# Optimization experiments

Measured on AMD Instinct MI355X. Metric: run time of the kernel, lower is better.

## Reference

```python
import jax, jax.numpy as jnp
import numpy as np

T, B, HIMG = 16, 1024, 32
VALUE_DIM, KEY_DIM, HIDDEN, OUT_DIM = 64, 64, 512, 4


def _conv(x, w):
    # torch Conv2d(kernel=4, stride=2, padding=0)
    return jax.lax.conv_general_dilated(
        x, w, (2, 2), 'VALID', dimension_numbers=('NCHW', 'OIHW', 'NCHW'))


def setup_inputs() -> dict:
    key = jax.random.key(0)
    ks = jax.random.split(key, 24)

    def w(k, shape, s=0.05):
        return jax.random.normal(k, shape, jnp.float32) * s

    return {
        'images': jax.random.normal(ks[0], (T, B, 3, HIMG, HIMG), jnp.float32),
        # encoder
        'W1': w(ks[1], (32, 3, 4, 4)), 'b1': w(ks[2], (32,)),
        'W2': w(ks[3], (64, 32, 4, 4)), 'b2': w(ks[4], (64,)),
        'W3': w(ks[5], (64, 64, 4, 4)), 'b3': w(ks[6], (64,)),
        'We': w(ks[7], (VALUE_DIM, 4 * 64)), 'be': w(ks[8], (VALUE_DIM,)),
        # LSTMCell(key_dim+1 -> hidden), torch layout (4H, in) / (4H, H)
        'Wih': w(ks[9], (4 * HIDDEN, KEY_DIM + 1)),
        'Whh': w(ks[10], (4 * HIDDEN, HIDDEN)),
        'bih': w(ks[11], (4 * HIDDEN,)), 'bhh': w(ks[12], (4 * HIDDEN,)),
        # heads
        'Wg': w(ks[13], (1, HIDDEN)), 'bg': w(ks[14], (1,)),
        'Wk': w(ks[15], (KEY_DIM, HIDDEN)), 'bk': w(ks[16], (KEY_DIM,)),
        'Wo': w(ks[17], (OUT_DIM, HIDDEN)), 'bo': w(ks[18], (OUT_DIM,)),
        'Wc': w(ks[19], (1, 1)), 'bc': w(ks[20], (1,)),
    }


def _forward(images, W1, b1, W2, b2, W3, b3, We, be,
             Wih, Whh, bih, bhh, Wg, bg, Wk, bk, Wo, bo, Wc, bc):
    t, b = images.shape[0], images.shape[1]

    # Encoder over all frames at once (vectorized over T*B).
    # FAITHFULNESS NOTE: in the source module, the retrieved key `kr` is computed
    # but never assigned back to `kx` (kx stays k0 = zeros after step 0), so the
    # encoder output z / memory banks Mk, Mv / gate / key / confidence heads never
    # influence the returned output. We compute z here to mirror the source; it is
    # dead w.r.t. the output (XLA will DCE it under jit), exactly matching torch.
    x = images.reshape((t * b,) + images.shape[2:])
    h = jax.nn.relu(_conv(x, W1) + b1[None, :, None, None])
    h = jax.nn.relu(_conv(h, W2) + b2[None, :, None, None])
    h = jax.nn.relu(_conv(h, W3) + b3[None, :, None, None])
    z = h.reshape(t * b, -1) @ We.T + be  # (t*b, value_dim) -- dead path
    del z

    hidden = Whh.shape[1]
    kx = jnp.zeros((b, Wih.shape[1]), images.dtype)  # k0; constant every step (source bug)
    const_gates = kx @ Wih.T + bih + bhh             # (b, 4*hidden), hoisted out of the loop

    def step(carry, _):
        hx, cx = carry
        gates = const_gates + hx @ Whh.T
        i, f, g, o = jnp.split(gates, 4, axis=-1)  # torch LSTMCell gate order i,f,g,o
        cx = jax.nn.sigmoid(f) * cx + jax.nn.sigmoid(i) * jnp.tanh(g)
        hx = jax.nn.sigmoid(o) * jnp.tanh(cx)
        return (hx, cx), hx

    init = (jnp.zeros((b, hidden), images.dtype),
            jnp.zeros((b, hidden), images.dtype))
    _, hs = jax.lax.scan(step, init, None, length=t)  # (t, b, hidden)
    return hs @ Wo.T + bo  # (t, b, output_dim) == torch.stack(out)


def reference(images, W1, b1, W2, b2, W3, b3, We, be,
              Wih, Whh, bih, bhh, Wg, bg, Wk, bk, Wo, bo, Wc, bc):
    return _forward(images, W1, b1, W2, b2, W3, b3, We, be,
                    Wih, Whh, bih, bhh, Wg, bg, Wk, bk, Wo, bo, Wc, bc)
```

## Files before the change

kernel.cpp:

```cpp
#include <hip/hip_runtime.h>


#define NTHR   512
#define HID    512
#define TSTEPS 16
#define KPB    16
#define OUTB   16
#define NWORK  32
#define SW     516

typedef unsigned long long ull;

#define LOG2E  1.44269504f

__device__ __forceinline__ float fexp2(float x) { return __builtin_amdgcn_exp2f(x); }
__device__ __forceinline__ float frcp(float x)  { return __builtin_amdgcn_rcpf(x); }
__device__ __forceinline__ float sigm(float x)  { return frcp(1.0f + fexp2(-LOG2E * x)); }
__device__ __forceinline__ float tanh_f(float x) {
  const float e = fexp2(2.0f * LOG2E * x);
  return 1.0f - 2.0f * frcp(e + 1.0f);
}

__device__ __forceinline__ ull probe_l2(const ull* p) {
  ull v;
  asm volatile("global_load_dwordx2 %0, %1, off sc0\n\ts_waitcnt vmcnt(0)"
               : "=v"(v) : "v"(p) : "memory");
  return v;
}

__device__ __forceinline__ float poll_h(const ull* sL2, const ull* sLLC,
                                        int idx, unsigned tag, bool fast) {
  ull v;
  if (fast) {
    for (;;) {
      v = probe_l2(sL2 + idx);
      if ((unsigned)(v >> 32) == tag) break;
      v = __hip_atomic_load(sLLC + idx, __ATOMIC_RELAXED,
                            __HIP_MEMORY_SCOPE_AGENT);
      if ((unsigned)(v >> 32) == tag) break;
    }
  } else {
    do {
      v = __hip_atomic_load(sLLC + idx, __ATOMIC_RELAXED,
                            __HIP_MEMORY_SCOPE_AGENT);
    } while ((unsigned)(v >> 32) != tag);
  }
  return __uint_as_float((unsigned)v);
}

__device__ __forceinline__ void publish(ull* sL2, ull* sLLC, int idx, ull pk,
                                        bool fast) {
  if (fast) {
    asm volatile("global_store_dwordx2 %0, %1, off sc0"
                 :: "v"(sL2 + idx), "v"(pk) : "memory");
  }
  __hip_atomic_store(sLLC + idx, pk, __ATOMIC_RELAXED, __HIP_MEMORY_SCOPE_AGENT);
}

__global__ __launch_bounds__(NTHR, 2) void lstm_seq_kernel(
    const float* __restrict__ Whh,
    const float* __restrict__ bih,
    const float* __restrict__ bhh,
    const float* __restrict__ Wo,
    const float* __restrict__ bo,
    float* __restrict__ out,
    ull* sLLC,
    ull* sL2,
    int mode)
{
  int r;
  if (mode) {
    if (blockIdx.x & 7) return;
    r = (int)(blockIdx.x >> 3);
  } else {
    r = (int)blockIdx.x;
  }
  if (r >= NWORK) return;
  const bool fast = (mode != 0);

  const int tid = threadIdx.x;
  const int w  = tid >> 6;
  const int l  = tid & 63;
  const int grow = (l >> 4) * HID + r * KPB + (l & 15);

  __shared__ float ldsw[64 * SW];
  __shared__ __align__(16) float chbuf[8][64];
  __shared__ float gpT[2][8][64];
  __shared__ float hstash[HID];
  __shared__ float vals[4];

#pragma unroll
  for (int g4 = 0; g4 < 4; ++g4) {
    const float* base = Whh + ((size_t)g4 * HID + (size_t)r * KPB) * HID;
#pragma unroll
    for (int it = 0; it < 4; ++it) {
      const int flat = it * 2048 + tid * 4;
      const float4 v = *reinterpret_cast<const float4*>(base + flat);
      const int rw = flat >> 9;
      const int cl = flat & 511;
      *reinterpret_cast<float4*>(&ldsw[(g4 * 16 + rw) * SW + cl]) = v;
    }
  }

  {
    const float gi = bih[tid]           + bhh[tid];
    const float gf = bih[HID + tid]     + bhh[HID + tid];
    const float gg = bih[2*HID + tid]   + bhh[2*HID + tid];
    const float go = bih[3*HID + tid]   + bhh[3*HID + tid];
    const float c1 = sigm(gf) * 0.0f + sigm(gi) * tanh_f(gg);
    const float h1 = sigm(go) * tanh_f(c1);
    chbuf[w][l] = h1;
    if (r == 0) hstash[tid] = h1;
  }

  float c_state = 0.0f;
  float bias_row = 0.0f;
  if (w == 0) bias_row = bih[grow] + bhh[grow];
  if (tid < KPB) {
    const int k = r * KPB + tid;
    const float bs_i = bih[k]           + bhh[k];
    const float bs_f = bih[HID + k]     + bhh[HID + k];
    const float bs_g = bih[2*HID + k]   + bhh[2*HID + k];
    c_state = sigm(bs_f) * 0.0f + sigm(bs_i) * tanh_f(bs_g);
  }

  __syncthreads();

  float4 wreg[16];
#pragma unroll
  for (int j = 0; j < 16; ++j)
    wreg[j] = *reinterpret_cast<const float4*>(&ldsw[l * SW + w * 64 + j * 4]);

  for (int s = 2; s <= TSTEPS; ++s) {
    const int p = s & 1;

    float4 a = make_float4(0.f, 0.f, 0.f, 0.f);
    {
      const float4* hq = reinterpret_cast<const float4*>(&chbuf[w][0]);
#pragma unroll
      for (int j = 0; j < 16; ++j) {
        const float4 h4 = hq[j];
        a.x = fmaf(wreg[j].x, h4.x, a.x);
        a.y = fmaf(wreg[j].y, h4.y, a.y);
        a.z = fmaf(wreg[j].z, h4.z, a.z);
        a.w = fmaf(wreg[j].w, h4.w, a.w);
      }
    }
    gpT[p][w][l] = (a.x + a.y) + (a.z + a.w);
    __syncthreads();

    if (w == 0) {
      float d = gpT[p][0][l];
#pragma unroll
      for (int j = 1; j < 8; ++j) d += gpT[p][j][l];
      d += bias_row;
      const float gf = __shfl_xor(d, 16);
      const float gg = __shfl_xor(d, 32);
      const float go = __shfl_xor(d, 48);
      if (l < KPB) {
        c_state = sigm(gf) * c_state + sigm(d) * tanh_f(gg);
        const float hv = sigm(go) * tanh_f(c_state);
        const ull pk = ((ull)(unsigned)s << 32) | (ull)__float_as_uint(hv);
        publish(sL2, sLLC, p * HID + r * KPB + l, pk, fast);
      }
    }

    if (s < TSTEPS) {
      const float h = poll_h(sL2, sLLC, p * HID + w * 64 + l, (unsigned)s, fast);
      if (r >= 1 && r < OUTB - 1 && s == r + 1) hstash[w * 64 + l] = h;
      chbuf[w][l] = h;
    }
  }

  if (r >= OUTB) return;

  if (r == OUTB - 1) {
    hstash[w * 64 + l] = poll_h(sL2, sLLC, w * 64 + l, (unsigned)TSTEPS, fast);
  }
  __syncthreads();

  if (tid < 256) {
    const int wo = tid >> 6;
    const int ll = tid & 63;
    float sacc = 0.0f;
#pragma unroll
    for (int j = 0; j < 8; ++j) {
      const int k2 = ll + 64 * j;
      sacc = fmaf(Wo[wo * HID + k2], hstash[k2], sacc);
    }
#pragma unroll
    for (int m = 32; m > 0; m >>= 1) sacc += __shfl_xor(sacc, m);
    if (ll == 0) vals[wo] = sacc + bo[wo];
  }
  __syncthreads();

  const float4 vv = make_float4(vals[0], vals[1], vals[2], vals[3]);
  float4* out4 = reinterpret_cast<float4*>(out) + (size_t)r * 1024;
  out4[tid]       = vv;
  out4[tid + 512] = vv;
}

extern "C" void kernel_launch(void* const* d_in, const int* in_sizes, int n_in,
                              void* d_out, int out_size, void* d_ws, size_t ws_size,
                              hipStream_t stream) {
  const float* Whh = (const float*)d_in[10];
  const float* bih = (const float*)d_in[11];
  const float* bhh = (const float*)d_in[12];
  const float* Wo  = (const float*)d_in[17];
  const float* bo  = (const float*)d_in[18];
  float* out = (float*)d_out;

  ull* sLLC; ull* sL2; int mode; int grid;
  if (d_ws != nullptr && ws_size >= 4 * HID * sizeof(ull)) {
    sLLC = (ull*)d_ws;
    sL2  = sLLC + 2 * HID;
    mode = 1;
    grid = NWORK * 8;
  } else {
    sLLC = (ull*)(out + (size_t)out_size) - 2 * HID;
    sL2  = sLLC;
    mode = 0;
    grid = NWORK;
  }

  lstm_seq_kernel<<<dim3(grid), dim3(NTHR), 0, stream>>>(
      Whh, bih, bhh, Wo, bo, out, sLLC, sL2, mode);
}
```

Measured before the change: 26.56 us.

## Replace dual-slot L2/LLC polling with single atomic-exchange slot and compact grid

Drops the fast mode, which launched 8x blocks so the 32 workers would land on separate XCDs and published to both an L2-cached slot and an LLC slot. Now exactly 32 blocks are launched and each publishes its hidden values with a device-scope atomic exchange followed by a wait, while readers poll a single slot with relaxed agent-scope loads. This is meant to cut the duplicate stores and the two-stage probe loop in the cross-block step barrier. In exchange, blocks may now share an XCD or not, and the atomic round trip plus the explicit wait adds latency to each publish.

```diff
diff --git a/kernel.cpp b/kernel.cpp
--- a/kernel.cpp
+++ b/kernel.cpp
@@ -21,40 +21,19 @@
   return 1.0f - 2.0f * frcp(e + 1.0f);
 }
 
-__device__ __forceinline__ ull probe_l2(const ull* p) {
+__device__ __forceinline__ float poll_h(const ull* slots, int idx, unsigned tag) {
   ull v;
-  asm volatile("global_load_dwordx2 %0, %1, off sc0\n\ts_waitcnt vmcnt(0)"
-               : "=v"(v) : "v"(p) : "memory");
-  return v;
-}
-
-__device__ __forceinline__ float poll_h(const ull* sL2, const ull* sLLC,
-                                        int idx, unsigned tag, bool fast) {
-  ull v;
-  if (fast) {
-    for (;;) {
-      v = probe_l2(sL2 + idx);
-      if ((unsigned)(v >> 32) == tag) break;
-      v = __hip_atomic_load(sLLC + idx, __ATOMIC_RELAXED,
-                            __HIP_MEMORY_SCOPE_AGENT);
-      if ((unsigned)(v >> 32) == tag) break;
-    }
-  } else {
-    do {
-      v = __hip_atomic_load(sLLC + idx, __ATOMIC_RELAXED,
-                            __HIP_MEMORY_SCOPE_AGENT);
-    } while ((unsigned)(v >> 32) != tag);
-  }
+  do {
+    v = __hip_atomic_load(slots + idx, __ATOMIC_RELAXED,
+                          __HIP_MEMORY_SCOPE_AGENT);
+  } while ((unsigned)(v >> 32) != tag);
   return __uint_as_float((unsigned)v);
 }
 
-__device__ __forceinline__ void publish(ull* sL2, ull* sLLC, int idx, ull pk,
-                                        bool fast) {
-  if (fast) {
-    asm volatile("global_store_dwordx2 %0, %1, off sc0"
-                 :: "v"(sL2 + idx), "v"(pk) : "memory");
-  }
-  __hip_atomic_store(sLLC + idx, pk, __ATOMIC_RELAXED, __HIP_MEMORY_SCOPE_AGENT);
+__device__ __forceinline__ void publish(ull* slots, int idx, ull pk) {
+  (void)__hip_atomic_exchange(slots + idx, pk, __ATOMIC_RELAXED,
+                              __HIP_MEMORY_SCOPE_AGENT);
+  asm volatile("s_waitcnt vmcnt(0)" ::: "memory");
 }
 
 __global__ __launch_bounds__(NTHR, 2) void lstm_seq_kernel(
@@ -64,20 +43,9 @@
     const float* __restrict__ Wo,
     const float* __restrict__ bo,
     float* __restrict__ out,
-    ull* sLLC,
-    ull* sL2,
-    int mode)
+    ull* slots)
 {
-  int r;
-  if (mode) {
-    if (blockIdx.x & 7) return;
-    r = (int)(blockIdx.x >> 3);
-  } else {
-    r = (int)blockIdx.x;
-  }
-  if (r >= NWORK) return;
-  const bool fast = (mode != 0);
-
+  const int r = (int)blockIdx.x;
   const int tid = threadIdx.x;
   const int w  = tid >> 6;
   const int l  = tid & 63;
@@ -161,12 +129,12 @@
         c_state = sigm(gf) * c_state + sigm(d) * tanh_f(gg);
         const float hv = sigm(go) * tanh_f(c_state);
         const ull pk = ((ull)(unsigned)s << 32) | (ull)__float_as_uint(hv);
-        publish(sL2, sLLC, p * HID + r * KPB + l, pk, fast);
+        publish(slots, p * HID + r * KPB + l, pk);
       }
     }
 
     if (s < TSTEPS) {
-      const float h = poll_h(sL2, sLLC, p * HID + w * 64 + l, (unsigned)s, fast);
+      const float h = poll_h(slots, p * HID + w * 64 + l, (unsigned)s);
       if (r >= 1 && r < OUTB - 1 && s == r + 1) hstash[w * 64 + l] = h;
       chbuf[w][l] = h;
     }
@@ -175,7 +143,7 @@
   if (r >= OUTB) return;
 
   if (r == OUTB - 1) {
-    hstash[w * 64 + l] = poll_h(sL2, sLLC, w * 64 + l, (unsigned)TSTEPS, fast);
+    hstash[w * 64 + l] = poll_h(slots, w * 64 + l, (unsigned)TSTEPS);
   }
   __syncthreads();
 
@@ -210,19 +178,13 @@
   const float* bo  = (const float*)d_in[18];
   float* out = (float*)d_out;
 
-  ull* sLLC; ull* sL2; int mode; int grid;
-  if (d_ws != nullptr && ws_size >= 4 * HID * sizeof(ull)) {
-    sLLC = (ull*)d_ws;
-    sL2  = sLLC + 2 * HID;
-    mode = 1;
-    grid = NWORK * 8;
+  ull* slots;
+  if (d_ws != nullptr && ws_size >= 2 * HID * sizeof(ull)) {
+    slots = (ull*)d_ws;
   } else {
-    sLLC = (ull*)(out + (size_t)out_size) - 2 * HID;
-    sL2  = sLLC;
-    mode = 0;
-    grid = NWORK;
+    slots = (ull*)(out + (size_t)out_size) - 2 * HID;
   }
 
-  lstm_seq_kernel<<<dim3(grid), dim3(NTHR), 0, stream>>>(
-      Whh, bih, bhh, Wo, bo, out, sLLC, sL2, mode);
+  lstm_seq_kernel<<<dim3(NWORK), dim3(NTHR), 0, stream>>>(
+      Whh, bih, bhh, Wo, bo, out, slots);
 }
```

New measurement: 30.52 us. 1.15x slower.
